# Optimization experiments

Measured on AMD Instinct MI355X. Metric: run time of the kernel, lower is better.

## Reference

```python
import jax, jax.numpy as jnp
import numpy as np

B, T, C = 8, 4096, 768


def wkv(w, u, k, v):
    """RWKV WKV linear recurrence with running max/exp state.
    w, u: (C,) ; k, v: (B, T, C) -> y: (B, T, C), all float32.
    Faithful to wkv_pytorch: note w is ADDED to pp (no negation/exp).
    """
    kt = jnp.swapaxes(k, 0, 1)  # (T, B, C)
    vt = jnp.swapaxes(v, 0, 1)

    def step(carry, inp):
        aa, bb, pp = carry            # each (B, C)
        k_t, v_t = inp                # each (B, C)
        ww = u[None, :] + k_t
        p = jnp.maximum(pp, ww)
        e1 = jnp.exp(pp - p)
        e2 = jnp.exp(ww - p)
        y_t = (e1 * aa + e2 * v_t) / (e1 * bb + e2)
        ww2 = w[None, :] + pp
        p2 = jnp.maximum(ww2, k_t)
        e1b = jnp.exp(ww2 - p2)
        e2b = jnp.exp(k_t - p2)
        aa = e1b * aa + e2b * v_t
        bb = e1b * bb + e2b
        return (aa, bb, p2), y_t

    init = (jnp.zeros((B, C), jnp.float32),
            jnp.zeros((B, C), jnp.float32),
            jnp.full((B, C), -1e38, jnp.float32))
    _, y = jax.lax.scan(step, init, (kt, vt))
    return jnp.swapaxes(y, 0, 1)  # (B, T, C)


def setup_inputs() -> dict:
    key = jax.random.key(0)
    ks = jax.random.split(key, 7)
    scale = 1.0 / np.sqrt(C)
    x = jax.random.normal(ks[0], (B, T, C), jnp.float32)
    w_key = jax.random.normal(ks[1], (C, C), jnp.float32) * scale
    w_value = jax.random.normal(ks[2], (C, C), jnp.float32) * scale
    w_receptance = jax.random.normal(ks[3], (C, C), jnp.float32) * scale
    w_output = jax.random.normal(ks[4], (C, C), jnp.float32) * scale
    # 'fancy' init, layer_id=5, n_layer=12
    layer_id, n_layer = 5, 12
    ratio_0_to_1 = layer_id / (n_layer - 1)
    h = np.arange(C, dtype=np.float64)
    spatial_decay = (-5.0 + 8.0 * (h / (C - 1)) ** (0.7 + 1.3 * ratio_0_to_1)).astype(np.float32)
    zigzag = (np.array([(i + 1) % 3 - 1 for i in range(C)], dtype=np.float64) * 0.5)
    spatial_first = (np.ones(C) * np.log(0.3) + zigzag).astype(np.float32)
    return {
        "x": x,
        "w_key": w_key,
        "w_value": w_value,
        "w_receptance": w_receptance,
        "w_output": w_output,
        "spatial_decay": jnp.asarray(spatial_decay),
        "spatial_first": jnp.asarray(spatial_first),
    }


def reference(x, w_key, w_value, w_receptance, w_output, spatial_decay, spatial_first):
    # shift_pixel=0, empty spatial_shift_list -> xk = xv = xr = x
    k = jnp.einsum('btc,oc->bto', x, w_key)
    v = jnp.einsum('btc,oc->bto', x, w_value)
    sr = jax.nn.sigmoid(jnp.einsum('btc,oc->bto', x, w_receptance))
    y = wkv(spatial_decay / T, spatial_first / T, k, v)
    out = jnp.einsum('btc,oc->bto', sr * y, w_output)
    return out
```

## Files before the change

kernel.cpp:

```cpp
#include <hip/hip_runtime.h>
#include <hip/hip_bf16.h>

using bf16 = __hip_bfloat16;
typedef short bf16x8v  __attribute__((ext_vector_type(8)));
typedef float f32x16v  __attribute__((ext_vector_type(16)));

#define GLD_LDS16(g, l) __builtin_amdgcn_global_load_lds(                      \
    (const __attribute__((address_space(1))) void*)(g),                        \
    (__attribute__((address_space(3))) void*)(l), 16, 0, 0)

__device__ __forceinline__ float bflo(unsigned int u) {
  union { unsigned int i; float f; } c; c.i = u << 16; return c.f;
}
__device__ __forceinline__ float bfhi(unsigned int u) {
  union { unsigned int i; float f; } c; c.i = u & 0xffff0000u; return c.f;
}
__device__ __forceinline__ unsigned int packbf(float a, float b) {
  return (unsigned int)(__hip_bfloat16_raw(__float2bfloat16(a)).x) |
         ((unsigned int)(__hip_bfloat16_raw(__float2bfloat16(b)).x) << 16);
}
__device__ __forceinline__ unsigned short bfraw(float a) {
  return __hip_bfloat16_raw(__float2bfloat16(a)).x;
}

__global__ void f2b4_all(const float* __restrict__ x,  const float* __restrict__ wk,
                         const float* __restrict__ wv, const float* __restrict__ wr,
                         const float* __restrict__ wo,
                         bf16* __restrict__ x_bf, bf16* __restrict__ wcat,
                         bf16* __restrict__ wo_bf) {
  int i = blockIdx.x * blockDim.x + threadIdx.x;
  const float* s; bf16* d; int idx;
  if (i < 6291456) { s = x; d = x_bf; idx = i; }
  else {
    int j = i - 6291456;
    int seg = j / 147456;
    idx = j - seg * 147456;
    if (seg == 0)      { s = wk; d = wcat; }
    else if (seg == 1) { s = wv; d = wcat + 589824; }
    else if (seg == 2) { s = wr; d = wcat + 1179648; }
    else               { s = wo; d = wo_bf; }
  }
  const float4 f = reinterpret_cast<const float4*>(s)[idx];
  struct B4 { bf16 a, b, c, d; };
  B4 o = { __float2bfloat16(f.x), __float2bfloat16(f.y),
           __float2bfloat16(f.z), __float2bfloat16(f.w) };
  reinterpret_cast<B4*>(d)[idx] = o;
}

__device__ __forceinline__ void gemm_tile_acc(
    const bf16* __restrict__ A, const bf16* __restrict__ W,
    bf16* lds_a, bf16* lds_b, int tid, size_t m0, int n0, f32x16v acc[2][2])
{
  const int lane = tid & 63;
  const int wave = tid >> 6;
  const int l31  = lane & 31;
  const int hi   = lane >> 5;
  const int wr   = (wave >> 1) * 64;
  const int wc   = (wave & 1) * 64;

  int srow[4], scol[4];
#pragma unroll
  for (int q = 0; q < 4; ++q) {
    const int s = tid + q * 256;
    srow[q] = s >> 3;
    scol[q] = (((s & 7) ^ (srow[q] & 7)) * 8);
  }

#pragma unroll
  for (int i = 0; i < 2; ++i)
#pragma unroll
    for (int j = 0; j < 2; ++j)
#pragma unroll
      for (int r = 0; r < 16; ++r) acc[i][j][r] = 0.0f;

  for (int k0 = 0; k0 < 768; k0 += 64) {
    __syncthreads();
#pragma unroll
    for (int q = 0; q < 4; ++q)
      GLD_LDS16(A + (m0 + srow[q]) * 768 + k0 + scol[q], &lds_a[(size_t)(tid + q * 256) * 8]);
#pragma unroll
    for (int q = 0; q < 4; ++q)
      GLD_LDS16(W + (size_t)(n0 + srow[q]) * 768 + k0 + scol[q], &lds_b[(size_t)(tid + q * 256) * 8]);
    __syncthreads();

#pragma unroll
    for (int ks = 0; ks < 4; ++ks) {
      const int gl = ks * 2 + hi;
      bf16x8v av[2], bv[2];
#pragma unroll
      for (int i = 0; i < 2; ++i) {
        const int ra = wr + 32 * i + l31;
        av[i] = *(const bf16x8v*)&lds_a[ra * 64 + ((gl ^ (ra & 7)) * 8)];
      }
#pragma unroll
      for (int j = 0; j < 2; ++j) {
        const int rb = wc + 32 * j + l31;
        bv[j] = *(const bf16x8v*)&lds_b[rb * 64 + ((gl ^ (rb & 7)) * 8)];
      }
#pragma unroll
      for (int i = 0; i < 2; ++i)
#pragma unroll
        for (int j = 0; j < 2; ++j)
          acc[i][j] = __builtin_amdgcn_mfma_f32_32x32x16_bf16(bv[j], av[i], acc[i][j], 0, 0, 0);
    }
  }
}


__global__ __launch_bounds__(256) void gemm_kvr(
    const bf16* __restrict__ A, const bf16* __restrict__ Wcat,
    bf16* __restrict__ Kb, bf16* __restrict__ Vb, bf16* __restrict__ SRb)
{
  __shared__ __align__(16) bf16 lds_a[128 * 64];
  __shared__ __align__(16) bf16 lds_b[128 * 64];
  const int tid = threadIdx.x;
  const int bx = blockIdx.x;
  const int chunk = bx / 1152;
  const int rem   = bx % 1152;
  const int mm    = rem & 63;
  const int nt    = rem >> 6;
  const size_t m0 = (size_t)(chunk * 64 + mm) * 128;
  const int n0 = nt * 128;

  f32x16v acc[2][2];
  gemm_tile_acc(A, Wcat, lds_a, lds_b, tid, m0, n0, acc);

  const int seg   = n0 / 768;
  const int ncol0 = n0 - seg * 768;
  bf16* __restrict__ dst = (seg == 0) ? Kb : (seg == 1) ? Vb : SRb;
  const int lane = tid & 63, wave = tid >> 6;
  const int l31 = lane & 31, hi = lane >> 5;
  const int wr = (wave >> 1) * 64, wc = (wave & 1) * 64;
#pragma unroll
  for (int i = 0; i < 2; ++i) {
    const size_t mrow = m0 + wr + 32 * i + l31;
#pragma unroll
    for (int j = 0; j < 2; ++j) {
      const int nb = ncol0 + wc + 32 * j + 4 * hi;
#pragma unroll
      for (int rr = 0; rr < 4; ++rr) {
        float v0 = acc[i][j][4 * rr + 0], v1 = acc[i][j][4 * rr + 1];
        float v2 = acc[i][j][4 * rr + 2], v3 = acc[i][j][4 * rr + 3];
        if (seg == 2) {
          v0 = 1.0f / (1.0f + __expf(-v0)); v1 = 1.0f / (1.0f + __expf(-v1));
          v2 = 1.0f / (1.0f + __expf(-v2)); v3 = 1.0f / (1.0f + __expf(-v3));
        }
        ushort4 pk = { bfraw(v0), bfraw(v1), bfraw(v2), bfraw(v3) };
        *(ushort4*)&dst[mrow * 768 + nb + 8 * rr] = pk;
      }
    }
  }
}

__global__ __launch_bounds__(256) void gemm_out(
    const bf16* __restrict__ A, const bf16* __restrict__ W,
    float* __restrict__ out)
{
  __shared__ __align__(16) bf16 lds_a[128 * 64];
  __shared__ __align__(16) bf16 lds_b[128 * 64];
  const int tid = threadIdx.x;
  const int bx = blockIdx.x;
  const int chunk = bx / 384;
  const int rem   = bx % 384;
  const int mm    = rem & 63;
  const int nt    = rem >> 6;
  const size_t m0 = (size_t)(chunk * 64 + mm) * 128;
  const int n0 = nt * 128;

  f32x16v acc[2][2];
  gemm_tile_acc(A, W, lds_a, lds_b, tid, m0, n0, acc);

  const int lane = tid & 63, wave = tid >> 6;
  const int l31 = lane & 31, hi = lane >> 5;
  const int wr = (wave >> 1) * 64, wc = (wave & 1) * 64;
#pragma unroll
  for (int i = 0; i < 2; ++i) {
    const size_t mrow = m0 + wr + 32 * i + l31;
#pragma unroll
    for (int j = 0; j < 2; ++j) {
      const int nb = n0 + wc + 32 * j + 4 * hi;
#pragma unroll
      for (int rr = 0; rr < 4; ++rr) {
        float4 pk = { acc[i][j][4 * rr + 0], acc[i][j][4 * rr + 1],
                      acc[i][j][4 * rr + 2], acc[i][j][4 * rr + 3] };
        *(float4*)&out[mrow * 768 + nb + 8 * rr] = pk;
      }
    }
  }
}

__global__ void wkv_phaseA(const bf16* __restrict__ K, const bf16* __restrict__ V,
                           const float* __restrict__ sd,
                           float* __restrict__ sA, float* __restrict__ sB, float* __restrict__ sP)
{
  const int idx = blockIdx.x * 256 + threadIdx.x;
  const int c4 = idx % 192;
  const int bg = idx / 192;
  const int g  = bg & 127;
  const int b  = bg >> 7;
  const int c0 = c4 * 4;
  float w[4], aa[4], bb[4], pp[4];
#pragma unroll
  for (int e = 0; e < 4; ++e) {
    w[e] = sd[c0 + e] * (1.0f / 4096.0f);
    aa[e] = 0.f; bb[e] = 0.f; pp[e] = -1e38f;
  }
  const size_t base = ((size_t)b * 4096 + (size_t)g * 32) * 768 + c0;
  const uint2* Kp = (const uint2*)(K + base);
  const uint2* Vp = (const uint2*)(V + base);
#pragma unroll 4
  for (int t = 0; t < 32; ++t) {
    const uint2 ku = Kp[(size_t)t * 192];
    const uint2 vu = Vp[(size_t)t * 192];
    const float kc[4] = { bflo(ku.x), bfhi(ku.x), bflo(ku.y), bfhi(ku.y) };
    const float vc[4] = { bflo(vu.x), bfhi(vu.x), bflo(vu.y), bfhi(vu.y) };
#pragma unroll
    for (int e = 0; e < 4; ++e) {
      const float ww2 = w[e] + pp[e];
      const float p2  = fmaxf(ww2, kc[e]);
      const float e1b = __expf(ww2 - p2);
      const float e2b = __expf(kc[e] - p2);
      aa[e] = e1b * aa[e] + e2b * vc[e];
      bb[e] = e1b * bb[e] + e2b;
      pp[e] = p2;
    }
  }
  const int o = g * 6144 + b * 768 + c0;
#pragma unroll
  for (int e = 0; e < 4; ++e) { sA[o + e] = aa[e]; sB[o + e] = bb[e]; sP[o + e] = pp[e]; }
}

__global__ void wkv_phaseB(const float* __restrict__ sA, const float* __restrict__ sB,
                           const float* __restrict__ sP,
                           float* __restrict__ iA, float* __restrict__ iB, float* __restrict__ iP,
                           const float* __restrict__ sd)
{
  const int bc = blockIdx.x * 256 + threadIdx.x;
  const int c  = bc % 768;
  const float Lw = 32.0f * (sd[c] * (1.0f / 4096.0f));
  float aa = 0.f, bb = 0.f, pp = -1e38f;
  for (int g = 0; g < 128; ++g) {
    const int o = g * 6144 + bc;
    iA[o] = aa; iB[o] = bb; iP[o] = pp;
    const float la = sA[o], lb = sB[o], lp = sP[o];
    const float pd = pp + Lw;
    const float pn = fmaxf(pd, lp);
    const float e0 = __expf(pd - pn);
    const float e1 = __expf(lp - pn);
    aa = e0 * aa + e1 * la;
    bb = e0 * bb + e1 * lb;
    pp = pn;
  }
}

__global__ void wkv_phaseC(const bf16* __restrict__ K, const bf16* __restrict__ V,
                           const bf16* __restrict__ SR,
                           const float* __restrict__ iA, const float* __restrict__ iB,
                           const float* __restrict__ iP,
                           const float* __restrict__ sd, const float* __restrict__ sf,
                           bf16* __restrict__ RY)
{
  const int idx = blockIdx.x * 256 + threadIdx.x;
  const int c4 = idx % 192;
  const int bg = idx / 192;
  const int g  = bg & 127;
  const int b  = bg >> 7;
  const int c0 = c4 * 4;
  const int o = g * 6144 + b * 768 + c0;
  float w[4], u[4], aa[4], bb[4], pp[4];
#pragma unroll
  for (int e = 0; e < 4; ++e) {
    w[e] = sd[c0 + e] * (1.0f / 4096.0f);
    u[e] = sf[c0 + e] * (1.0f / 4096.0f);
    aa[e] = iA[o + e]; bb[e] = iB[o + e]; pp[e] = iP[o + e];
  }
  const size_t base = ((size_t)b * 4096 + (size_t)g * 32) * 768 + c0;
  const uint2* Kp = (const uint2*)(K + base);
  const uint2* Vp = (const uint2*)(V + base);
  const uint2* Sp = (const uint2*)(SR + base);
  uint2* Rp = (uint2*)(RY + base);
#pragma unroll 4
  for (int t = 0; t < 32; ++t) {
    const uint2 ku = Kp[(size_t)t * 192];
    const uint2 vu = Vp[(size_t)t * 192];
    const uint2 su = Sp[(size_t)t * 192];
    const float kc[4] = { bflo(ku.x), bfhi(ku.x), bflo(ku.y), bfhi(ku.y) };
    const float vc[4] = { bflo(vu.x), bfhi(vu.x), bflo(vu.y), bfhi(vu.y) };
    const float sc[4] = { bflo(su.x), bfhi(su.x), bflo(su.y), bfhi(su.y) };
    float y[4];
#pragma unroll
    for (int e = 0; e < 4; ++e) {
      const float ww = u[e] + kc[e];
      const float p  = fmaxf(pp[e], ww);
      const float e1 = __expf(pp[e] - p);
      const float e2 = __expf(ww - p);
      y[e] = (e1 * aa[e] + e2 * vc[e]) / (e1 * bb[e] + e2) * sc[e];
      const float ww2 = w[e] + pp[e];
      const float p2  = fmaxf(ww2, kc[e]);
      const float e1b = __expf(ww2 - p2);
      const float e2b = __expf(kc[e] - p2);
      aa[e] = e1b * aa[e] + e2b * vc[e];
      bb[e] = e1b * bb[e] + e2b;
      pp[e] = p2;
    }
    uint2 r; r.x = packbf(y[0], y[1]); r.y = packbf(y[2], y[3]);
    Rp[(size_t)t * 192] = r;
  }
}

extern "C" void kernel_launch(void* const* d_in, const int* in_sizes, int n_in,
                              void* d_out, int out_size, void* d_ws, size_t ws_size,
                              hipStream_t stream)
{
  const float* x  = (const float*)d_in[0];
  const float* wk = (const float*)d_in[1];
  const float* wv = (const float*)d_in[2];
  const float* wr = (const float*)d_in[3];
  const float* wo = (const float*)d_in[4];
  const float* sd = (const float*)d_in[5];
  const float* sf = (const float*)d_in[6];
  float* out = (float*)d_out;

  char* ws = (char*)d_ws;
  bf16*  x_bf  = (bf16*) (ws + 0);
  bf16*  wcat  = (bf16*) (ws + 50331648);
  bf16*  wo_bf = (bf16*) (ws + 53870592);
  bf16*  Kb    = (bf16*) (ws + 55050240);
  bf16*  Vb    = (bf16*) (ws + 105381888);
  bf16*  SRb   = (bf16*) (ws + 155713536);
  float* sumA  = (float*)(ws + 206045184);
  float* sumB  = (float*)(ws + 209190912);
  float* sumP  = (float*)(ws + 212336640);
  float* iniA  = (float*)(ws + 215482368);
  float* iniB  = (float*)(ws + 218628096);
  float* iniP  = (float*)(ws + 221773824);
  bf16*  ry_bf = x_bf;

  f2b4_all<<<26880, 256, 0, stream>>>(x, wk, wv, wr, wo, x_bf, wcat, wo_bf);

  gemm_kvr<<<4608, 256, 0, stream>>>(x_bf, wcat, Kb, Vb, SRb);

  wkv_phaseA<<<768, 256, 0, stream>>>(Kb, Vb, sd, sumA, sumB, sumP);
  wkv_phaseB<<<24,  256, 0, stream>>>(sumA, sumB, sumP, iniA, iniB, iniP, sd);
  wkv_phaseC<<<768, 256, 0, stream>>>(Kb, Vb, SRb, iniA, iniB, iniP, sd, sf, ry_bf);

  gemm_out<<<1536, 256, 0, stream>>>(ry_bf, wo_bf, out);
}
```

Measured before the change: 475.4 us.

## Rewrite GEMMs as 256x256 double-buffered tiles with phased MFMA scheduling

Both GEMMs move from 128x128 tiles with 4 waves and a single LDS buffer to 256x256 tiles with 8 waves and double-buffered LDS. Global-to-LDS loads for the next K slab are interleaved with MFMA phases, using explicit vmcnt waits, barriers and s_setprio to overlap memory with compute. Block indices are remapped (XCD-style swizzle) so neighbouring tiles share operands in cache. This raises data reuse per tile and hides load latency. The cost is 128KB of LDS per block and higher register pressure, and the hand-ordered waitcnt sequence is fragile.

```diff
diff --git a/kernel.cpp b/kernel.cpp
--- a/kernel.cpp
+++ b/kernel.cpp
@@ -47,96 +47,181 @@
   reinterpret_cast<B4*>(d)[idx] = o;
 }
 
-__device__ __forceinline__ void gemm_tile_acc(
+
+__device__ __forceinline__ void stg(bf16* dst, const bf16* src, int kt,
+                                    const int srow[2], const int scol[2],
+                                    int tid) {
+#pragma unroll
+  for (int q = 0; q < 2; ++q)
+    GLD_LDS16(src + (size_t)srow[q] * 768 + kt * 64 + scol[q],
+              dst + (size_t)(tid + q * 512) * 8);
+}
+
+__device__ __forceinline__ void lda2(bf16x8v av[2][4], const bf16* bufA,
+                                     int aBase, int ih, int hi, int sx) {
+#pragma unroll
+  for (int ks = 0; ks < 4; ++ks)
+#pragma unroll
+    for (int ii = 0; ii < 2; ++ii)
+      av[ii][ks] = *(const bf16x8v*)(bufA + aBase + (ih * 2 + ii) * 2048 +
+                                     (((ks * 2 + hi) ^ sx) * 8));
+}
+
+__device__ __forceinline__ void ldb1(bf16x8v bv[4], const bf16* bufB,
+                                     int bBase, int j, int hi, int sx) {
+#pragma unroll
+  for (int ks = 0; ks < 4; ++ks)
+    bv[ks] = *(const bf16x8v*)(bufB + bBase + j * 2048 +
+                               (((ks * 2 + hi) ^ sx) * 8));
+}
+
+__device__ __forceinline__ void mm8(f32x16v acc[4][2], const bf16x8v av[2][4],
+                                    const bf16x8v bv[4], int ih, int j) {
+#pragma unroll
+  for (int ks = 0; ks < 4; ++ks)
+#pragma unroll
+    for (int ii = 0; ii < 2; ++ii)
+      acc[ih * 2 + ii][j] = __builtin_amdgcn_mfma_f32_32x32x16_bf16(
+          bv[ks], av[ii][ks], acc[ih * 2 + ii][j], 0, 0, 0);
+}
+
+#define PH_SYNC_PRE()                                                          \
+  __builtin_amdgcn_s_barrier();                                                \
+  asm volatile("s_waitcnt lgkmcnt(0)" ::: "memory");                           \
+  __builtin_amdgcn_s_setprio(1);
+
+#define PH_SYNC_POST()                                                         \
+  __builtin_amdgcn_s_setprio(0);                                               \
+  __builtin_amdgcn_s_barrier();
+
+__device__ __forceinline__ void gemm256_core(
     const bf16* __restrict__ A, const bf16* __restrict__ W,
-    bf16* lds_a, bf16* lds_b, int tid, size_t m0, int n0, f32x16v acc[2][2])
-{
-  const int lane = tid & 63;
-  const int wave = tid >> 6;
-  const int l31  = lane & 31;
-  const int hi   = lane >> 5;
-  const int wr   = (wave >> 1) * 64;
-  const int wc   = (wave & 1) * 64;
-
-  int srow[4], scol[4];
-#pragma unroll
-  for (int q = 0; q < 4; ++q) {
-    const int s = tid + q * 256;
+    bf16* lds, size_t m0, size_t n0, int tid, f32x16v acc[4][2])
+{
+  bf16* const A0 = lds;
+  bf16* const B0 = lds + 16384;
+  bf16* const A1 = lds + 32768;
+  bf16* const B1 = lds + 49152;
+
+  const int lane = tid & 63, wave = tid >> 6;
+  const int l31 = lane & 31, hi = lane >> 5;
+  const int wm = wave >> 2, wn = wave & 3;
+  const int sx = l31 & 7;
+  const int aBase = (wm * 128 + l31) * 64;
+  const int bBase = (wn * 64 + l31) * 64;
+
+  int srow[2], scol[2];
+#pragma unroll
+  for (int q = 0; q < 2; ++q) {
+    const int s = tid + q * 512;
     srow[q] = s >> 3;
-    scol[q] = (((s & 7) ^ (srow[q] & 7)) * 8);
-  }
-
-#pragma unroll
-  for (int i = 0; i < 2; ++i)
+    scol[q] = ((s & 7) ^ (srow[q] & 7)) * 8;
+  }
+  const bf16* aS0 = A + m0 * 768;
+  const bf16* aS1 = A + (m0 + 128) * 768;
+  const bf16* bS0 = W + n0 * 768;
+  const bf16* bS1 = W + (n0 + 128) * 768;
+
+  bf16x8v av[2][4], bv[2][4];
+
+#pragma unroll
+  for (int i = 0; i < 4; ++i)
 #pragma unroll
     for (int j = 0; j < 2; ++j)
 #pragma unroll
       for (int r = 0; r < 16; ++r) acc[i][j][r] = 0.0f;
 
-  for (int k0 = 0; k0 < 768; k0 += 64) {
-    __syncthreads();
-#pragma unroll
-    for (int q = 0; q < 4; ++q)
-      GLD_LDS16(A + (m0 + srow[q]) * 768 + k0 + scol[q], &lds_a[(size_t)(tid + q * 256) * 8]);
-#pragma unroll
-    for (int q = 0; q < 4; ++q)
-      GLD_LDS16(W + (size_t)(n0 + srow[q]) * 768 + k0 + scol[q], &lds_b[(size_t)(tid + q * 256) * 8]);
-    __syncthreads();
-
-#pragma unroll
-    for (int ks = 0; ks < 4; ++ks) {
-      const int gl = ks * 2 + hi;
-      bf16x8v av[2], bv[2];
-#pragma unroll
-      for (int i = 0; i < 2; ++i) {
-        const int ra = wr + 32 * i + l31;
-        av[i] = *(const bf16x8v*)&lds_a[ra * 64 + ((gl ^ (ra & 7)) * 8)];
-      }
-#pragma unroll
-      for (int j = 0; j < 2; ++j) {
-        const int rb = wc + 32 * j + l31;
-        bv[j] = *(const bf16x8v*)&lds_b[rb * 64 + ((gl ^ (rb & 7)) * 8)];
-      }
-#pragma unroll
-      for (int i = 0; i < 2; ++i)
-#pragma unroll
-        for (int j = 0; j < 2; ++j)
-          acc[i][j] = __builtin_amdgcn_mfma_f32_32x32x16_bf16(bv[j], av[i], acc[i][j], 0, 0, 0);
+  stg(A0,        aS0, 0, srow, scol, tid);
+  stg(A0 + 8192, aS1, 0, srow, scol, tid);
+  stg(B0,        bS0, 0, srow, scol, tid);
+  stg(B0 + 8192, bS1, 0, srow, scol, tid);
+  stg(B1,        bS0, 1, srow, scol, tid);
+  stg(B1 + 8192, bS1, 1, srow, scol, tid);
+  asm volatile("s_waitcnt vmcnt(4)" ::: "memory");
+  __builtin_amdgcn_s_barrier();
+
+  for (int it = 0; it < 6; ++it) {
+    const bool last = (it == 5);
+    const int ta = 2 * it + 1;
+    const int tb = 2 * it + 2;
+    const int tc = 2 * it + 3;
+
+    lda2(av, A0, aBase, 0, hi, sx);
+    ldb1(bv[0], B0, bBase, 0, hi, sx);
+    stg(A1, aS0, ta, srow, scol, tid);
+    PH_SYNC_PRE(); mm8(acc, av, bv[0], 0, 0); PH_SYNC_POST();
+
+    ldb1(bv[1], B0, bBase, 1, hi, sx);
+    stg(A1 + 8192, aS1, ta, srow, scol, tid);
+    PH_SYNC_PRE(); mm8(acc, av, bv[1], 0, 1); PH_SYNC_POST();
+
+    lda2(av, A0, aBase, 1, hi, sx);
+    if (!last) stg(B0, bS0, tb, srow, scol, tid);
+    PH_SYNC_PRE(); mm8(acc, av, bv[0], 1, 0); PH_SYNC_POST();
+
+    if (!last) stg(B0 + 8192, bS1, tb, srow, scol, tid);
+    __builtin_amdgcn_s_barrier();
+    __builtin_amdgcn_s_setprio(1);
+    mm8(acc, av, bv[1], 1, 1);
+    __builtin_amdgcn_s_setprio(0);
+    if (last) asm volatile("s_waitcnt vmcnt(0)" ::: "memory");
+    else      asm volatile("s_waitcnt vmcnt(4)" ::: "memory");
+    __builtin_amdgcn_s_barrier();
+
+    lda2(av, A1, aBase, 0, hi, sx);
+    ldb1(bv[0], B1, bBase, 0, hi, sx);
+    if (!last) stg(A0, aS0, tb, srow, scol, tid);
+    PH_SYNC_PRE(); mm8(acc, av, bv[0], 0, 0); PH_SYNC_POST();
+
+    ldb1(bv[1], B1, bBase, 1, hi, sx);
+    if (!last) stg(A0 + 8192, aS1, tb, srow, scol, tid);
+    PH_SYNC_PRE(); mm8(acc, av, bv[1], 0, 1); PH_SYNC_POST();
+
+    lda2(av, A1, aBase, 1, hi, sx);
+    if (!last) stg(B1, bS0, tc, srow, scol, tid);
+    PH_SYNC_PRE(); mm8(acc, av, bv[0], 1, 0); PH_SYNC_POST();
+
+    if (!last) stg(B1 + 8192, bS1, tc, srow, scol, tid);
+    __builtin_amdgcn_s_barrier();
+    __builtin_amdgcn_s_setprio(1);
+    mm8(acc, av, bv[1], 1, 1);
+    __builtin_amdgcn_s_setprio(0);
+    if (!last) {
+      asm volatile("s_waitcnt vmcnt(4)" ::: "memory");
+      __builtin_amdgcn_s_barrier();
     }
   }
 }
 
 
-__global__ __launch_bounds__(256) void gemm_kvr(
+__global__ __launch_bounds__(512, 2) void gemm_kvr(
     const bf16* __restrict__ A, const bf16* __restrict__ Wcat,
     bf16* __restrict__ Kb, bf16* __restrict__ Vb, bf16* __restrict__ SRb)
 {
-  __shared__ __align__(16) bf16 lds_a[128 * 64];
-  __shared__ __align__(16) bf16 lds_b[128 * 64];
+  __shared__ __align__(16) bf16 lds[65536];
   const int tid = threadIdx.x;
-  const int bx = blockIdx.x;
-  const int chunk = bx / 1152;
-  const int rem   = bx % 1152;
-  const int mm    = rem & 63;
-  const int nt    = rem >> 6;
-  const size_t m0 = (size_t)(chunk * 64 + mm) * 128;
-  const int n0 = nt * 128;
-
-  f32x16v acc[2][2];
-  gemm_tile_acc(A, Wcat, lds_a, lds_b, tid, m0, n0, acc);
-
-  const int seg   = n0 / 768;
+  const int bid = blockIdx.x;
+  const int tl  = (bid & 7) * 144 + (bid >> 3);
+  const int mt  = tl / 9;
+  const int ntl = tl - mt * 9;
+  const size_t m0 = (size_t)mt * 256;
+  const int n0 = ntl * 256;
+
+  f32x16v acc[4][2];
+  gemm256_core(A, Wcat, lds, m0, (size_t)n0, tid, acc);
+
+  const int seg   = (n0 >= 1536) ? 2 : (n0 >= 768) ? 1 : 0;
   const int ncol0 = n0 - seg * 768;
   bf16* __restrict__ dst = (seg == 0) ? Kb : (seg == 1) ? Vb : SRb;
   const int lane = tid & 63, wave = tid >> 6;
   const int l31 = lane & 31, hi = lane >> 5;
-  const int wr = (wave >> 1) * 64, wc = (wave & 1) * 64;
-#pragma unroll
-  for (int i = 0; i < 2; ++i) {
-    const size_t mrow = m0 + wr + 32 * i + l31;
+  const int wm = wave >> 2, wn = wave & 3;
+#pragma unroll
+  for (int i = 0; i < 4; ++i) {
+    const size_t mrow = m0 + wm * 128 + 32 * i + l31;
 #pragma unroll
     for (int j = 0; j < 2; ++j) {
-      const int nb = ncol0 + wc + 32 * j + 4 * hi;
+      const int nb = ncol0 + wn * 64 + 32 * j + 4 * hi;
 #pragma unroll
       for (int rr = 0; rr < 4; ++rr) {
         float v0 = acc[i][j][4 * rr + 0], v1 = acc[i][j][4 * rr + 1];
@@ -152,33 +237,31 @@
   }
 }
 
-__global__ __launch_bounds__(256) void gemm_out(
+__global__ __launch_bounds__(512, 2) void gemm_out(
     const bf16* __restrict__ A, const bf16* __restrict__ W,
     float* __restrict__ out)
 {
-  __shared__ __align__(16) bf16 lds_a[128 * 64];
-  __shared__ __align__(16) bf16 lds_b[128 * 64];
+  __shared__ __align__(16) bf16 lds[65536];
   const int tid = threadIdx.x;
-  const int bx = blockIdx.x;
-  const int chunk = bx / 384;
-  const int rem   = bx % 384;
-  const int mm    = rem & 63;
-  const int nt    = rem >> 6;
-  const size_t m0 = (size_t)(chunk * 64 + mm) * 128;
-  const int n0 = nt * 128;
-
-  f32x16v acc[2][2];
-  gemm_tile_acc(A, W, lds_a, lds_b, tid, m0, n0, acc);
+  const int bid = blockIdx.x;
+  const int tl  = (bid & 7) * 48 + (bid >> 3);
+  const int mt  = tl / 3;
+  const int ntl = tl - mt * 3;
+  const size_t m0 = (size_t)mt * 256;
+  const int n0 = ntl * 256;
+
+  f32x16v acc[4][2];
+  gemm256_core(A, W, lds, m0, (size_t)n0, tid, acc);
 
   const int lane = tid & 63, wave = tid >> 6;
   const int l31 = lane & 31, hi = lane >> 5;
-  const int wr = (wave >> 1) * 64, wc = (wave & 1) * 64;
-#pragma unroll
-  for (int i = 0; i < 2; ++i) {
-    const size_t mrow = m0 + wr + 32 * i + l31;
+  const int wm = wave >> 2, wn = wave & 3;
+#pragma unroll
+  for (int i = 0; i < 4; ++i) {
+    const size_t mrow = m0 + wm * 128 + 32 * i + l31;
 #pragma unroll
     for (int j = 0; j < 2; ++j) {
-      const int nb = n0 + wc + 32 * j + 4 * hi;
+      const int nb = n0 + wn * 64 + 32 * j + 4 * hi;
 #pragma unroll
       for (int rr = 0; rr < 4; ++rr) {
         float4 pk = { acc[i][j][4 * rr + 0], acc[i][j][4 * rr + 1],
@@ -338,11 +421,11 @@
 
   f2b4_all<<<26880, 256, 0, stream>>>(x, wk, wv, wr, wo, x_bf, wcat, wo_bf);
 
-  gemm_kvr<<<4608, 256, 0, stream>>>(x_bf, wcat, Kb, Vb, SRb);
+  gemm_kvr<<<1152, 512, 0, stream>>>(x_bf, wcat, Kb, Vb, SRb);
 
   wkv_phaseA<<<768, 256, 0, stream>>>(Kb, Vb, sd, sumA, sumB, sumP);
   wkv_phaseB<<<24,  256, 0, stream>>>(sumA, sumB, sumP, iniA, iniB, iniP, sd);
   wkv_phaseC<<<768, 256, 0, stream>>>(Kb, Vb, SRb, iniA, iniB, iniP, sd, sf, ry_bf);
 
-  gemm_out<<<1536, 256, 0, stream>>>(ry_bf, wo_bf, out);
-}
+  gemm_out<<<384, 512, 0, stream>>>(ry_bf, wo_bf, out);
+}
```

New measurement: 471.0 us. No clear change (-0.9%).

## Double-buffer GEMM LDS tiles with BK=32 and prefetch phaseB scan loads

Applied to the files above, without the earlier changes.

The shared GEMM mainloop now uses two 32-wide K stages held in ping-pong LDS buffers, with a new swizzle. The global-to-LDS load of the next stage is issued before the MFMAs on the current stage, so each K step needs one barrier instead of two. Separately, the phaseB scan launches 96 blocks of 64 threads instead of 24 blocks of 256 to spread across more CUs, and it software-prefetches the next group's partial sums. The tradeoffs are twice as many K iterations, and waiting on vmcnt(0) right after compute, which may limit how much load latency is actually hidden.

```diff
diff --git a/kernel.cpp b/kernel.cpp
--- a/kernel.cpp
+++ b/kernel.cpp
@@ -47,10 +47,57 @@
   reinterpret_cast<B4*>(d)[idx] = o;
 }
 
+__device__ __forceinline__ void stage32(
+    const bf16* __restrict__ A, const bf16* __restrict__ W,
+    bf16* lds_a, bf16* lds_b, int k0, size_t m0, int n0,
+    const int srow[2], const int scol[2], int tid)
+{
+#pragma unroll
+  for (int q = 0; q < 2; ++q) {
+    GLD_LDS16(A + (m0 + srow[q]) * 768 + k0 + scol[q],
+              &lds_a[(size_t)(tid + q * 256) * 8]);
+    GLD_LDS16(W + ((size_t)n0 + srow[q]) * 768 + k0 + scol[q],
+              &lds_b[(size_t)(tid + q * 256) * 8]);
+  }
+}
+
+__device__ __forceinline__ void comp32(
+    const bf16* lds_a, const bf16* lds_b, int wr, int wc, int l31, int hi,
+    f32x16v acc[2][2])
+{
+#pragma unroll
+  for (int ks = 0; ks < 2; ++ks) {
+    const int gl = ks * 2 + hi;
+    bf16x8v av[2], bv[2];
+#pragma unroll
+    for (int i = 0; i < 2; ++i) {
+      const int ra = wr + 32 * i + l31;
+      av[i] = *(const bf16x8v*)&lds_a[(ra >> 1) * 64 + (ra & 1) * 32 +
+                                      ((gl ^ ((ra >> 1) & 3)) * 8)];
+    }
+#pragma unroll
+    for (int j = 0; j < 2; ++j) {
+      const int rb = wc + 32 * j + l31;
+      bv[j] = *(const bf16x8v*)&lds_b[(rb >> 1) * 64 + (rb & 1) * 32 +
+                                      ((gl ^ ((rb >> 1) & 3)) * 8)];
+    }
+#pragma unroll
+    for (int i = 0; i < 2; ++i)
+#pragma unroll
+      for (int j = 0; j < 2; ++j)
+        acc[i][j] = __builtin_amdgcn_mfma_f32_32x32x16_bf16(bv[j], av[i], acc[i][j], 0, 0, 0);
+  }
+}
+
 __device__ __forceinline__ void gemm_tile_acc(
     const bf16* __restrict__ A, const bf16* __restrict__ W,
-    bf16* lds_a, bf16* lds_b, int tid, size_t m0, int n0, f32x16v acc[2][2])
-{
+    bf16* lds, int tid, size_t m0, int n0, f32x16v acc[2][2])
+{
+  bf16* const a0 = lds;
+  bf16* const b0 = lds + 4096;
+  bf16* const a1 = lds + 8192;
+  bf16* const b1 = lds + 12288;
+
   const int lane = tid & 63;
   const int wave = tid >> 6;
   const int l31  = lane & 31;
@@ -58,12 +105,12 @@
   const int wr   = (wave >> 1) * 64;
   const int wc   = (wave & 1) * 64;
 
-  int srow[4], scol[4];
-#pragma unroll
-  for (int q = 0; q < 4; ++q) {
+  int srow[2], scol[2];
+#pragma unroll
+  for (int q = 0; q < 2; ++q) {
     const int s = tid + q * 256;
-    srow[q] = s >> 3;
-    scol[q] = (((s & 7) ^ (srow[q] & 7)) * 8);
+    srow[q] = 2 * (s >> 3) + ((s >> 2) & 1);
+    scol[q] = ((s & 3) ^ ((s >> 3) & 3)) * 8;
   }
 
 #pragma unroll
@@ -73,35 +120,22 @@
 #pragma unroll
       for (int r = 0; r < 16; ++r) acc[i][j][r] = 0.0f;
 
-  for (int k0 = 0; k0 < 768; k0 += 64) {
-    __syncthreads();
-#pragma unroll
-    for (int q = 0; q < 4; ++q)
-      GLD_LDS16(A + (m0 + srow[q]) * 768 + k0 + scol[q], &lds_a[(size_t)(tid + q * 256) * 8]);
-#pragma unroll
-    for (int q = 0; q < 4; ++q)
-      GLD_LDS16(W + (size_t)(n0 + srow[q]) * 768 + k0 + scol[q], &lds_b[(size_t)(tid + q * 256) * 8]);
-    __syncthreads();
-
-#pragma unroll
-    for (int ks = 0; ks < 4; ++ks) {
-      const int gl = ks * 2 + hi;
-      bf16x8v av[2], bv[2];
-#pragma unroll
-      for (int i = 0; i < 2; ++i) {
-        const int ra = wr + 32 * i + l31;
-        av[i] = *(const bf16x8v*)&lds_a[ra * 64 + ((gl ^ (ra & 7)) * 8)];
-      }
-#pragma unroll
-      for (int j = 0; j < 2; ++j) {
-        const int rb = wc + 32 * j + l31;
-        bv[j] = *(const bf16x8v*)&lds_b[rb * 64 + ((gl ^ (rb & 7)) * 8)];
-      }
-#pragma unroll
-      for (int i = 0; i < 2; ++i)
-#pragma unroll
-        for (int j = 0; j < 2; ++j)
-          acc[i][j] = __builtin_amdgcn_mfma_f32_32x32x16_bf16(bv[j], av[i], acc[i][j], 0, 0, 0);
+  stage32(A, W, a0, b0, 0, m0, n0, srow, scol, tid);
+  asm volatile("s_waitcnt vmcnt(0)" ::: "memory");
+  __builtin_amdgcn_s_barrier();
+
+  for (int t = 0; t < 24; t += 2) {
+    stage32(A, W, a1, b1, (t + 1) * 32, m0, n0, srow, scol, tid);
+    comp32(a0, b0, wr, wc, l31, hi, acc);
+    asm volatile("s_waitcnt vmcnt(0)" ::: "memory");
+    __builtin_amdgcn_s_barrier();
+    if (t < 22) {
+      stage32(A, W, a0, b0, (t + 2) * 32, m0, n0, srow, scol, tid);
+      comp32(a1, b1, wr, wc, l31, hi, acc);
+      asm volatile("s_waitcnt vmcnt(0)" ::: "memory");
+      __builtin_amdgcn_s_barrier();
+    } else {
+      comp32(a1, b1, wr, wc, l31, hi, acc);
     }
   }
 }
@@ -111,8 +145,7 @@
     const bf16* __restrict__ A, const bf16* __restrict__ Wcat,
     bf16* __restrict__ Kb, bf16* __restrict__ Vb, bf16* __restrict__ SRb)
 {
-  __shared__ __align__(16) bf16 lds_a[128 * 64];
-  __shared__ __align__(16) bf16 lds_b[128 * 64];
+  __shared__ __align__(16) bf16 lds[16384];
   const int tid = threadIdx.x;
   const int bx = blockIdx.x;
   const int chunk = bx / 1152;
@@ -123,7 +156,7 @@
   const int n0 = nt * 128;
 
   f32x16v acc[2][2];
-  gemm_tile_acc(A, Wcat, lds_a, lds_b, tid, m0, n0, acc);
+  gemm_tile_acc(A, Wcat, lds, tid, m0, n0, acc);
 
   const int seg   = n0 / 768;
   const int ncol0 = n0 - seg * 768;
@@ -156,8 +189,7 @@
     const bf16* __restrict__ A, const bf16* __restrict__ W,
     float* __restrict__ out)
 {
-  __shared__ __align__(16) bf16 lds_a[128 * 64];
-  __shared__ __align__(16) bf16 lds_b[128 * 64];
+  __shared__ __align__(16) bf16 lds[16384];
   const int tid = threadIdx.x;
   const int bx = blockIdx.x;
   const int chunk = bx / 384;
@@ -168,7 +200,7 @@
   const int n0 = nt * 128;
 
   f32x16v acc[2][2];
-  gemm_tile_acc(A, W, lds_a, lds_b, tid, m0, n0, acc);
+  gemm_tile_acc(A, W, lds, tid, m0, n0, acc);
 
   const int lane = tid & 63, wave = tid >> 6;
   const int l31 = lane & 31, hi = lane >> 5;
@@ -235,14 +267,16 @@
                            float* __restrict__ iA, float* __restrict__ iB, float* __restrict__ iP,
                            const float* __restrict__ sd)
 {
-  const int bc = blockIdx.x * 256 + threadIdx.x;
+  const int bc = blockIdx.x * 64 + threadIdx.x;
   const int c  = bc % 768;
   const float Lw = 32.0f * (sd[c] * (1.0f / 4096.0f));
   float aa = 0.f, bb = 0.f, pp = -1e38f;
+  float la = sA[bc], lb = sB[bc], lp = sP[bc];
   for (int g = 0; g < 128; ++g) {
     const int o = g * 6144 + bc;
+    float la2 = 0.f, lb2 = 0.f, lp2 = 0.f;
+    if (g < 127) { la2 = sA[o + 6144]; lb2 = sB[o + 6144]; lp2 = sP[o + 6144]; }
     iA[o] = aa; iB[o] = bb; iP[o] = pp;
-    const float la = sA[o], lb = sB[o], lp = sP[o];
     const float pd = pp + Lw;
     const float pn = fmaxf(pd, lp);
     const float e0 = __expf(pd - pn);
@@ -250,6 +284,7 @@
     aa = e0 * aa + e1 * la;
     bb = e0 * bb + e1 * lb;
     pp = pn;
+    la = la2; lb = lb2; lp = lp2;
   }
 }
 
@@ -341,7 +376,7 @@
   gemm_kvr<<<4608, 256, 0, stream>>>(x_bf, wcat, Kb, Vb, SRb);
 
   wkv_phaseA<<<768, 256, 0, stream>>>(Kb, Vb, sd, sumA, sumB, sumP);
-  wkv_phaseB<<<24,  256, 0, stream>>>(sumA, sumB, sumP, iniA, iniB, iniP, sd);
+  wkv_phaseB<<<96,  64, 0, stream>>>(sumA, sumB, sumP, iniA, iniB, iniP, sd);
   wkv_phaseC<<<768, 256, 0, stream>>>(Kb, Vb, SRb, iniA, iniB, iniP, sd, sf, ry_bf);
 
   gemm_out<<<1536, 256, 0, stream>>>(ry_bf, wo_bf, out);
```

New measurement: 534.1 us. +12.4%, slower.
